# Kernel tuning notes

Hardware: AMD Instinct MI355X
Metric: run time of the kernel (lower is better)

Reference implementation:

```python
import jax, jax.numpy as jnp
import numpy as np

B, S, D, H, HD = 2, 2048, 1024, 16, 64
DFF = 4 * D
EPS = 1e-6


def _rms(x, w):
    return w * (x * jax.lax.rsqrt(jnp.mean(x * x, axis=-1, keepdims=True) + EPS))


def _rope(x, rope):
    # x: [B, H, S, HD], rope: [S, HD, 2]
    cos = rope[..., 0][None, None]
    sin = rope[..., 1][None, None]
    xr = x.reshape(*x.shape[:-1], -1, 2)
    rot = jnp.stack([-xr[..., 1], xr[..., 0]], axis=-1).reshape(x.shape)
    return x * cos + rot * sin


def setup_inputs() -> dict:
    key = jax.random.key(0)
    ks = jax.random.split(key, 10)
    w = lambda k, shape: jax.random.normal(k, shape, jnp.float32) * 0.02
    return {
        "hidden_states": jax.random.normal(ks[0], (B, S, D), jnp.float32),
        "timestep": jax.random.normal(ks[1], (B, D), jnp.float32),
        "rope_pos_embed": jax.random.normal(ks[2], (S, HD, 2), jnp.float32),
        "adaln_w": w(ks[3], (6 * D, D)),
        "adaln_b": jnp.zeros((6 * D,), jnp.float32),
        "wq": w(ks[4], (D, D)),
        "wk": w(ks[5], (D, D)),
        "wv": w(ks[6], (D, D)),
        "wo": w(ks[7], (D, D)),
        "q_norm_w": jnp.ones((D,), jnp.float32),
        "k_norm_w": jnp.ones((D,), jnp.float32),
        "norm3_w": jnp.ones((D,), jnp.float32),
        "fc1_w": w(ks[8], (DFF, D)),
        "fc1_b": jnp.zeros((DFF,), jnp.float32),
        "fc2_w": w(ks[9], (D, DFF)),
        "fc2_b": jnp.zeros((D,), jnp.float32),
    }


def reference(hidden_states, timestep, rope_pos_embed, adaln_w, adaln_b,
              wq, wk, wv, wo, q_norm_w, k_norm_w, norm3_w,
              fc1_w, fc1_b, fc2_w, fc2_b):
    x = hidden_states  # [B, S, D]
    # AdaLayerNorm: emb = Linear(SiLU(timestep)) -> 6 modulation chunks, broadcast over seq
    emb = jax.nn.silu(timestep) @ adaln_w.T + adaln_b  # [B, 6D]
    sh_msa, sc_msa, g_msa, sh_mlp, sc_mlp, g_mlp = jnp.split(emb[:, None, :], 6, axis=-1)
    mu = jnp.mean(x, axis=-1, keepdims=True)
    var = jnp.mean((x - mu) ** 2, axis=-1, keepdims=True)
    ln = (x - mu) * jax.lax.rsqrt(var + EPS)
    xm = ln * (1.0 + sc_msa) + sh_msa  # modulated input to attention

    # Attention: projections + RMSNorm over inner_dim + RoPE + SDPA
    q = _rms(xm @ wq.T, q_norm_w)
    k = _rms(xm @ wk.T, k_norm_w)
    v = xm @ wv.T
    q = q.reshape(B, S, H, HD).transpose(0, 2, 1, 3)
    k = k.reshape(B, S, H, HD).transpose(0, 2, 1, 3)
    v = v.reshape(B, S, H, HD).transpose(0, 2, 1, 3)
    q = _rope(q, rope_pos_embed)
    k = _rope(k, rope_pos_embed)
    scores = jnp.einsum('bhqd,bhkd->bhqk', q, k) * (HD ** -0.5)
    attn = jax.nn.softmax(scores, axis=-1)
    o = jnp.einsum('bhqk,bhkd->bhqd', attn, v)
    o = o.transpose(0, 2, 1, 3).reshape(B, S, H * HD) @ wo.T

    h = x + g_msa * o  # gated residual

    # MLP branch with AdaLN scale/shift on RMSNorm output
    n3 = _rms(h, norm3_w)
    nm = n3 * (1.0 + sc_mlp) + sh_mlp
    ff = jax.nn.gelu(nm @ fc1_w.T + fc1_b, approximate=True) @ fc2_w.T + fc2_b
    return h + g_mlp * ff
```

## Files before the change

kernel.cpp:

```cpp
#include <hip/hip_runtime.h>
#include <cstdint>
#include <cstddef>

typedef unsigned short ushort_t;
typedef __attribute__((ext_vector_type(8))) short s8v;
typedef __attribute__((ext_vector_type(4))) short s4v;
typedef __attribute__((ext_vector_type(4))) float f4v;

#define MFMA16(a, b, c) __builtin_amdgcn_mfma_f32_16x16x32_bf16(a, b, c, 0, 0, 0)

__device__ __forceinline__ ushort_t f2bf(float f) {
  union { float f; unsigned u; } a; a.f = f;
  return (ushort_t)((a.u + 0x7fffu + ((a.u >> 16) & 1u)) >> 16);
}
__device__ __forceinline__ float bf2f(ushort_t h) {
  union { unsigned u; float f; } a; a.u = ((unsigned)h) << 16; return a.f;
}
__device__ __forceinline__ unsigned fbits(float f) {
  union { float f; unsigned u; } a; a.f = f; return a.u;
}

__device__ __forceinline__ void gload16(const void* g, void* l) {
  __builtin_amdgcn_global_load_lds(
      (__attribute__((address_space(1))) void*)(uintptr_t)g,
      (__attribute__((address_space(3))) void*)(unsigned)(uintptr_t)l,
      16, 0, 0);
}

__launch_bounds__(256)
__global__ void convert_w(const float* __restrict__ wq, const float* __restrict__ wk,
                          const float* __restrict__ wv, const float* __restrict__ wo,
                          const float* __restrict__ f1, const float* __restrict__ f2,
                          ushort_t* __restrict__ dqkv, ushort_t* __restrict__ dwo,
                          ushort_t* __restrict__ df1, ushort_t* __restrict__ df2)
{
  const int blk = blockIdx.x;
  const float* src; ushort_t* dst; int off;
  if      (blk < 1024) { src = wq; dst = dqkv;            off = blk; }
  else if (blk < 2048) { src = wk; dst = dqkv + 1048576;  off = blk - 1024; }
  else if (blk < 3072) { src = wv; dst = dqkv + 2097152;  off = blk - 2048; }
  else if (blk < 4096) { src = wo; dst = dwo;             off = blk - 3072; }
  else if (blk < 8192) { src = f1; dst = df1;             off = blk - 4096; }
  else                 { src = f2; dst = df2;             off = blk - 8192; }
  const int idx = off * 1024 + threadIdx.x * 4;
  float4 v = *(const float4*)(src + idx);
  s4v o;
  o[0] = (short)f2bf(v.x); o[1] = (short)f2bf(v.y);
  o[2] = (short)f2bf(v.z); o[3] = (short)f2bf(v.w);
  *(s4v*)(dst + idx) = o;
}

__launch_bounds__(256)
__global__ void adaln(const float* __restrict__ ts, const float* __restrict__ w,
                      const float* __restrict__ bias, float* __restrict__ emb)
{
  const int j = blockIdx.x * 4 + (threadIdx.x >> 6);
  const int lane = threadIdx.x & 63;
  const float* wr = w + (size_t)j * 1024;
  float s0 = 0.f, s1 = 0.f;
  for (int i = lane; i < 1024; i += 64) {
    const float wv = wr[i];
    const float t0 = ts[i], t1 = ts[1024 + i];
    const float e0 = __builtin_amdgcn_exp2f(-1.4426950409f * t0);
    const float e1 = __builtin_amdgcn_exp2f(-1.4426950409f * t1);
    s0 += wv * t0 * __builtin_amdgcn_rcpf(1.f + e0);
    s1 += wv * t1 * __builtin_amdgcn_rcpf(1.f + e1);
  }
  #pragma unroll
  for (int m = 32; m; m >>= 1) { s0 += __shfl_down(s0, m); s1 += __shfl_down(s1, m); }
  if (!lane) { emb[j] = s0 + bias[j]; emb[6144 + j] = s1 + bias[j]; }
}

__launch_bounds__(256)
__global__ void ln_mod(const float* __restrict__ x, const float* __restrict__ emb,
                       ushort_t* __restrict__ xm)
{
  const int row = blockIdx.x, b = row >> 11, tid = threadIdx.x;
  const float* xr = x + (size_t)row * 1024;
  const int c = tid * 4;
  float4 v = *(const float4*)(xr + c);
  float s  = v.x + v.y + v.z + v.w;
  float s2 = v.x*v.x + v.y*v.y + v.z*v.z + v.w*v.w;
  #pragma unroll
  for (int m = 32; m; m >>= 1) { s += __shfl_down(s, m); s2 += __shfl_down(s2, m); }
  __shared__ float red[8];
  const int wave = tid >> 6, lane = tid & 63;
  if (!lane) { red[wave] = s; red[4 + wave] = s2; }
  __syncthreads();
  const float mu = (red[0] + red[1] + red[2] + red[3]) * (1.f / 1024.f);
  const float ms = (red[4] + red[5] + red[6] + red[7]) * (1.f / 1024.f);
  const float rstd = rsqrtf(ms - mu * mu + 1e-6f);
  const float* sh = emb + b * 6144;
  const float* sc = emb + b * 6144 + 1024;
  float4 shv = *(const float4*)(sh + c);
  float4 scv = *(const float4*)(sc + c);
  s4v ov;
  ov[0] = (short)f2bf((v.x - mu) * rstd * (1.f + scv.x) + shv.x);
  ov[1] = (short)f2bf((v.y - mu) * rstd * (1.f + scv.y) + shv.y);
  ov[2] = (short)f2bf((v.z - mu) * rstd * (1.f + scv.z) + shv.z);
  ov[3] = (short)f2bf((v.w - mu) * rstd * (1.f + scv.w) + shv.w);
  *(s4v*)(xm + (size_t)row * 1024 + c) = ov;
}

template<int EPI, int TN>
__launch_bounds__(256, 4)
__global__ void gemm_bt(const ushort_t* __restrict__ A, const ushort_t* __restrict__ Bw,
                        int K, int N,
                        ushort_t* __restrict__ outb, float* __restrict__ outf,
                        const float* __restrict__ bias, const float* __restrict__ resid,
                        const float* __restrict__ emb, int gate_off)
{
  constexpr int JN = TN / 32;
  constexpr int BUFB = TN * 32;
  __shared__ ushort_t As0[128 * 32], As1[128 * 32];
  __shared__ ushort_t Bs0[BUFB],    Bs1[BUFB];
  const int tid = threadIdx.x;
  const int wave = tid >> 6, lane = tid & 63;
  const int quad = lane >> 4, r = lane & 15;
  const int m0 = blockIdx.y * 128, n0 = blockIdx.x * TN;
  const int wm = (wave >> 1) * 64, wn = (wave & 1) * (TN / 2);

  const int srow = wave * 16 + (lane >> 2);
  const int scol = (lane & 3) * 8;
  const ushort_t* ag = A  + (size_t)(m0 + srow) * K + scol;
  const ushort_t* bg = Bw + (size_t)(n0 + srow) * K + scol;
  const size_t rowK64 = (size_t)64 * K;

  f4v acc[4][JN] = {};

  auto stage = [&](ushort_t* as, ushort_t* bs) {
    gload16(ag,          as + wave * 512);
    gload16(ag + rowK64, as + wave * 512 + 2048);
    gload16(bg,          bs + wave * 512);
    if (TN == 128) gload16(bg + rowK64, bs + wave * 512 + 2048);
    ag += 32; bg += 32;
  };
  auto compute = [&](const ushort_t* ab, const ushort_t* bb) {
    s8v af[4], bf[JN];
    #pragma unroll
    for (int i = 0; i < 4; i++)
      af[i] = *(const s8v*)(ab + (wm + i * 16 + r) * 32 + quad * 8);
    #pragma unroll
    for (int j = 0; j < JN; j++)
      bf[j] = *(const s8v*)(bb + (wn + j * 16 + r) * 32 + quad * 8);
    #pragma unroll
    for (int i = 0; i < 4; i++)
      #pragma unroll
      for (int j = 0; j < JN; j++)
        acc[i][j] = MFMA16(af[i], bf[j], acc[i][j]);
  };

  stage(As0, Bs0);
  __syncthreads();
  const int R = (K >> 6) - 1;
  for (int it = 0; it < R; it++) {
    stage(As1, Bs1);
    compute(As0, Bs0);
    __syncthreads();
    stage(As0, Bs0);
    compute(As1, Bs1);
    __syncthreads();
  }
  stage(As1, Bs1);
  compute(As0, Bs0);
  __syncthreads();
  compute(As1, Bs1);

  const int bblk = m0 >> 11;
  float bj[JN], gj[JN];
  #pragma unroll
  for (int j = 0; j < JN; j++) {
    const int col = n0 + wn + j * 16 + r;
    bj[j] = (EPI == 2 || EPI == 3) ? bias[col] : 0.f;
    gj[j] = (EPI == 1 || EPI == 3) ? emb[bblk * 6144 + gate_off + col] : 0.f;
  }
  #pragma unroll
  for (int i = 0; i < 4; i++) {
    #pragma unroll
    for (int rr = 0; rr < 4; rr++) {
      const int row = m0 + wm + i * 16 + quad * 4 + rr;
      const size_t rbase = (size_t)row * N + n0 + wn;
      #pragma unroll
      for (int j = 0; j < JN; j++) {
        float v = acc[i][j][rr];
        const size_t idx = rbase + j * 16 + r;
        if (EPI == 0) {
          outb[idx] = f2bf(v);
        } else if (EPI == 1) {
          outf[idx] = resid[idx] + gj[j] * v;
        } else if (EPI == 2) {
          v += bj[j];
          const float t = fmaf(v * v, 0.1029436f, 2.3022083f);
          const float e = __builtin_amdgcn_exp2f(-v * t);
          outb[idx] = f2bf(v * __builtin_amdgcn_rcpf(1.f + e));
        } else {
          outf[idx] = resid[idx] + gj[j] * (v + bj[j]);
        }
      }
    }
  }
}

__launch_bounds__(256)
__global__ void qkv_post(const ushort_t* __restrict__ qkv, const float* __restrict__ rope,
                         const float* __restrict__ qw, const float* __restrict__ kw,
                         ushort_t* __restrict__ q_r, ushort_t* __restrict__ k_r,
                         ushort_t* __restrict__ v_r)
{
  const int row = blockIdx.x, b = row >> 11, s = row & 2047, tid = threadIdx.x;
  const ushort_t* base = qkv + (size_t)row * 3072;
  const int c = tid * 4;
  s4v qv = *(const s4v*)(base + c);
  s4v kv = *(const s4v*)(base + 1024 + c);
  s4v vv = *(const s4v*)(base + 2048 + c);
  float qf[4], kf[4]; float sq = 0.f, sk = 0.f;
  #pragma unroll
  for (int i = 0; i < 4; i++) {
    qf[i] = bf2f((ushort_t)qv[i]); kf[i] = bf2f((ushort_t)kv[i]);
    sq += qf[i] * qf[i]; sk += kf[i] * kf[i];
  }
  #pragma unroll
  for (int m = 32; m; m >>= 1) { sq += __shfl_down(sq, m); sk += __shfl_down(sk, m); }
  __shared__ float red[8];
  const int wave = tid >> 6, lane = tid & 63;
  if (!lane) { red[wave] = sq; red[4 + wave] = sk; }
  __syncthreads();
  const float rq = rsqrtf((red[0]+red[1]+red[2]+red[3]) * (1.f/1024.f) + 1e-6f)
                   * 0.18033688011112042f;
  const float rk = rsqrtf((red[4]+red[5]+red[6]+red[7]) * (1.f/1024.f) + 1e-6f);

  const int h = c >> 6, d = c & 63;
  const float* rp = rope + ((size_t)s * 64 + d) * 2;
  float4 r01 = *(const float4*)(rp);
  float4 r23 = *(const float4*)(rp + 4);
  const float q0 = qf[0]*rq*qw[c], q1 = qf[1]*rq*qw[c+1];
  const float q2 = qf[2]*rq*qw[c+2], q3 = qf[3]*rq*qw[c+3];
  const float k0 = kf[0]*rk*kw[c], k1 = kf[1]*rk*kw[c+1];
  const float k2 = kf[2]*rk*kw[c+2], k3 = kf[3]*rk*kw[c+3];
  s4v qo, ko;
  qo[0] = (short)f2bf(q0 * r01.x - q1 * r01.y);
  qo[1] = (short)f2bf(q1 * r01.z + q0 * r01.w);
  qo[2] = (short)f2bf(q2 * r23.x - q3 * r23.y);
  qo[3] = (short)f2bf(q3 * r23.z + q2 * r23.w);
  ko[0] = (short)f2bf(k0 * r01.x - k1 * r01.y);
  ko[1] = (short)f2bf(k1 * r01.z + k0 * r01.w);
  ko[2] = (short)f2bf(k2 * r23.x - k3 * r23.y);
  ko[3] = (short)f2bf(k3 * r23.z + k2 * r23.w);
  const size_t rowbase = ((size_t)(b * 16 + h) * 2048 + s) * 64;
  const int d_s = (((d >> 3) ^ (s & 7)) << 3) | (d & 7);
  *(s4v*)(q_r + rowbase + d) = qo;
  *(s4v*)(k_r + rowbase + d_s) = ko;
  *(s4v*)(v_r + rowbase + d) = vv;
}

__launch_bounds__(256)
__global__ void vtrans(const ushort_t* __restrict__ v_r, ushort_t* __restrict__ v_t)
{
  const int bh = blockIdx.x >> 5, st = blockIdx.x & 31;
  const int s0 = st * 64;
  __shared__ ushort_t tile[64 * 72];
  const int tid = threadIdx.x;
  #pragma unroll
  for (int rep = 0; rep < 2; rep++) {
    const int idx = rep * 256 + tid;
    const int sr = idx >> 3, dc = (idx & 7) << 3;
    s8v val = *(const s8v*)(v_r + ((size_t)bh * 2048 + s0 + sr) * 64 + dc);
    *(s8v*)(tile + sr * 72 + dc) = val;
  }
  __syncthreads();
  #pragma unroll
  for (int rep = 0; rep < 2; rep++) {
    const int idx = rep * 256 + tid;
    const int d = idx >> 3;
    const int scs = (((idx & 7) ^ (d & 7)) << 3);
    s8v val;
    const int sc = (idx & 7) << 3;
    #pragma unroll
    for (int j = 0; j < 8; j++) val[j] = (short)tile[(sc + j) * 72 + d];
    *(s8v*)(v_t + ((size_t)bh * 64 + d) * 2048 + s0 + scs) = val;
  }
}

__launch_bounds__(256, 4)
__global__ void flash(const ushort_t* __restrict__ q_r, const ushort_t* __restrict__ k_r,
                      const ushort_t* __restrict__ v_t, ushort_t* __restrict__ attn)
{
  __shared__ ushort_t Ksh[2][64 * 64];
  __shared__ ushort_t Vsh[2][64 * 64];
  __shared__ ushort_t Psh[4][16 * 64];
  const int bh = blockIdx.x >> 5, qb = blockIdx.x & 31;
  const int tid = threadIdx.x, wave = tid >> 6, lane = tid & 63;
  const int quad = lane >> 4, r = lane & 15;
  const int rx = r & 7;
  const int q0 = qb * 64 + wave * 16;
  const size_t bhS = (size_t)bh * 2048;

  s8v aq0 = *(const s8v*)(q_r + (bhS + q0 + r) * 64 + quad * 8);
  s8v aq1 = *(const s8v*)(q_r + (bhS + q0 + r) * 64 + 32 + quad * 8);

  f4v o[4] = {};
  float mi = -1e30f, li = 0.f;

  const ushort_t* kg = k_r + (bhS + wave * 16 + (lane >> 3)) * 64 + (lane & 7) * 8;
  const ushort_t* vg = v_t + ((size_t)bh * 64 + wave * 16 + (lane >> 3)) * 2048
                       + (lane & 7) * 8;
  const int klo = wave * 1024 + lane * 8;
  const int vlo = wave * 1024 + lane * 8;
  ushort_t* pw = &Psh[wave][0];

  auto stage = [&](ushort_t* kbuf, ushort_t* vbuf, int kb) {
    #pragma unroll
    for (int c = 0; c < 2; c++) {
      gload16(kg + (size_t)(kb + c * 8) * 64, kbuf + klo + c * 512);
      gload16(vg + kb + (size_t)(c * 8) * 2048, vbuf + vlo + c * 512);
    }
  };

  auto step = [&](const ushort_t* Kc, const ushort_t* Vc) {
    f4v st[4];
    __builtin_amdgcn_s_setprio(1);
    #pragma unroll
    for (int t = 0; t < 4; t++) {
      const ushort_t* krow = Kc + (t * 16 + r) * 64;
      s8v k0 = *(const s8v*)(krow + ((quad ^ rx) << 3));
      s8v k1 = *(const s8v*)(krow + (((4 + quad) ^ rx) << 3));
      f4v z = {};
      z = MFMA16(k0, aq0, z);
      z = MFMA16(k1, aq1, z);
      st[t] = z;
    }
    __builtin_amdgcn_s_setprio(0);

    float m4[4];
    #pragma unroll
    for (int t = 0; t < 4; t++)
      m4[t] = fmaxf(fmaxf(st[t][0], st[t][1]), fmaxf(st[t][2], st[t][3]));
    float mloc = fmaxf(fmaxf(m4[0], m4[1]), fmaxf(m4[2], m4[3]));
    mloc = fmaxf(mloc, __shfl_xor(mloc, 16));
    mloc = fmaxf(mloc, __shfl_xor(mloc, 32));
    const float mn = fmaxf(mi, mloc);
    const float al = __builtin_amdgcn_exp2f(mi - mn);

    float p[4][4];
    uint2 pk[4];
    #pragma unroll
    for (int t = 0; t < 4; t++) {
      #pragma unroll
      for (int rr = 0; rr < 4; rr++)
        p[t][rr] = __builtin_amdgcn_exp2f(st[t][rr] - mn);
      const unsigned u0 = fbits(p[t][0]) + 0x8000u;
      const unsigned u1 = fbits(p[t][1]) + 0x8000u;
      const unsigned u2 = fbits(p[t][2]) + 0x8000u;
      const unsigned u3 = fbits(p[t][3]) + 0x8000u;
      pk[t].x = __builtin_amdgcn_perm(u1, u0, 0x07060302u);
      pk[t].y = __builtin_amdgcn_perm(u3, u2, 0x07060302u);
    }

    #pragma unroll
    for (int t = 0; t < 4; t++) {
      const int cw = t * 2 + (quad >> 1);
      const int sc = cw ^ rx;
      *(uint2*)(pw + r * 64 + (sc << 3) + (quad & 1) * 4) = pk[t];
    }

    float alo[4];
    #pragma unroll
    for (int rr = 0; rr < 4; rr++) alo[rr] = __shfl(al, quad * 4 + rr);
    #pragma unroll
    for (int nt = 0; nt < 4; nt++)
      #pragma unroll
      for (int rr = 0; rr < 4; rr++) o[nt][rr] *= alo[rr];

    float s4r[4];
    #pragma unroll
    for (int t = 0; t < 4; t++)
      s4r[t] = (p[t][0] + p[t][1]) + (p[t][2] + p[t][3]);
    float ls = (s4r[0] + s4r[1]) + (s4r[2] + s4r[3]);
    ls += __shfl_xor(ls, 16);
    ls += __shfl_xor(ls, 32);
    li = al * li + ls;
    mi = mn;

    asm volatile("s_waitcnt lgkmcnt(0)" ::: "memory");

    __builtin_amdgcn_s_setprio(1);
    #pragma unroll
    for (int kc = 0; kc < 2; kc++) {
      const int c = kc * 4 + quad;
      const int sc = c ^ rx;
      s8v ap = *(const s8v*)(pw + r * 64 + (sc << 3));
      #pragma unroll
      for (int nt = 0; nt < 4; nt++) {
        s8v bv = *(const s8v*)(Vc + (nt * 16 + r) * 64 + (sc << 3));
        o[nt] = MFMA16(ap, bv, o[nt]);
      }
    }
    __builtin_amdgcn_s_setprio(0);
  };

  stage(Ksh[0], Vsh[0], 0);
  __syncthreads();

  #pragma unroll 1
  for (int kb = 0; kb < 2048; kb += 128) {
    stage(Ksh[1], Vsh[1], kb + 64);
    step(Ksh[0], Vsh[0]);
    __syncthreads();
    if (kb + 128 < 2048) stage(Ksh[0], Vsh[0], kb + 128);
    step(Ksh[1], Vsh[1]);
    __syncthreads();
  }

  const int h = bh & 15, b = bh >> 4;
  const float linv = 1.f / li;
  #pragma unroll
  for (int rr = 0; rr < 4; rr++) {
    const float inv = __shfl(linv, quad * 4 + rr);
    const size_t orow = ((size_t)(b * 2048 + q0 + quad * 4 + rr)) * 1024 + h * 64;
    #pragma unroll
    for (int nt = 0; nt < 4; nt++)
      attn[orow + nt * 16 + r] = f2bf(o[nt][rr] * inv);
  }
}

__launch_bounds__(256)
__global__ void rms3_mod(const float* __restrict__ h, const float* __restrict__ emb,
                         const float* __restrict__ w3, ushort_t* __restrict__ nm)
{
  const int row = blockIdx.x, b = row >> 11, tid = threadIdx.x;
  const float* hr = h + (size_t)row * 1024;
  const int c = tid * 4;
  float4 v = *(const float4*)(hr + c);
  float s2 = v.x*v.x + v.y*v.y + v.z*v.z + v.w*v.w;
  #pragma unroll
  for (int m = 32; m; m >>= 1) s2 += __shfl_down(s2, m);
  __shared__ float red[4];
  const int wave = tid >> 6, lane = tid & 63;
  if (!lane) red[wave] = s2;
  __syncthreads();
  const float rms = rsqrtf((red[0] + red[1] + red[2] + red[3]) * (1.f / 1024.f) + 1e-6f);
  const float* sh = emb + b * 6144 + 3072;
  const float* sc = emb + b * 6144 + 4096;
  float4 shv = *(const float4*)(sh + c);
  float4 scv = *(const float4*)(sc + c);
  float4 wv  = *(const float4*)(w3 + c);
  s4v ov;
  ov[0] = (short)f2bf(v.x * rms * wv.x * (1.f + scv.x) + shv.x);
  ov[1] = (short)f2bf(v.y * rms * wv.y * (1.f + scv.y) + shv.y);
  ov[2] = (short)f2bf(v.z * rms * wv.z * (1.f + scv.z) + shv.z);
  ov[3] = (short)f2bf(v.w * rms * wv.w * (1.f + scv.w) + shv.w);
  *(s4v*)(nm + (size_t)row * 1024 + c) = ov;
}

extern "C" void kernel_launch(void* const* d_in, const int* in_sizes, int n_in,
                              void* d_out, int out_size, void* d_ws, size_t ws_size,
                              hipStream_t stream)
{
  const float* x    = (const float*)d_in[0];
  const float* ts   = (const float*)d_in[1];
  const float* rope = (const float*)d_in[2];
  const float* adw  = (const float*)d_in[3];
  const float* adb  = (const float*)d_in[4];
  const float* wq   = (const float*)d_in[5];
  const float* wk   = (const float*)d_in[6];
  const float* wv   = (const float*)d_in[7];
  const float* wo   = (const float*)d_in[8];
  const float* qnw  = (const float*)d_in[9];
  const float* knw  = (const float*)d_in[10];
  const float* n3w  = (const float*)d_in[11];
  const float* f1w  = (const float*)d_in[12];
  const float* f1b  = (const float*)d_in[13];
  const float* f2w  = (const float*)d_in[14];
  const float* f2b  = (const float*)d_in[15];

  char* ws = (char*)d_ws;
  ushort_t* WQKV = (ushort_t*)(ws + 0);
  ushort_t* WO   = (ushort_t*)(ws + 6291456);
  ushort_t* F1   = (ushort_t*)(ws + 8388608);
  ushort_t* F2   = (ushort_t*)(ws + 16777216);
  float*    EMB  = (float*)   (ws + 25165824);
  float*    H    = (float*)   (ws + 25214976);
  ushort_t* XM   = (ushort_t*)(ws + 41992192);
  ushort_t* QKV  = (ushort_t*)(ws + 50380800);
  ushort_t* QR   = (ushort_t*)(ws + 75546624);
  ushort_t* KR   = (ushort_t*)(ws + 83935232);
  ushort_t* VR   = (ushort_t*)(ws + 92323840);
  ushort_t* VT   = (ushort_t*)(ws + 100712448);
  ushort_t* ATTN = XM;
  ushort_t* NM   = QKV;
  ushort_t* FF1  = QR;

  convert_w<<<12288, 256, 0, stream>>>(wq, wk, wv, wo, f1w, f2w, WQKV, WO, F1, F2);
  adaln<<<1536, 256, 0, stream>>>(ts, adw, adb, EMB);
  ln_mod<<<4096, 256, 0, stream>>>(x, EMB, XM);
  gemm_bt<0, 128><<<dim3(24, 32), 256, 0, stream>>>(XM, WQKV, 1024, 3072,
      QKV, nullptr, nullptr, nullptr, nullptr, 0);
  qkv_post<<<4096, 256, 0, stream>>>(QKV, rope, qnw, knw, QR, KR, VR);
  vtrans<<<1024, 256, 0, stream>>>(VR, VT);
  flash<<<1024, 256, 0, stream>>>(QR, KR, VT, ATTN);
  gemm_bt<1, 64><<<dim3(16, 32), 256, 0, stream>>>(ATTN, WO, 1024, 1024,
      nullptr, H, nullptr, x, EMB, 2048);
  rms3_mod<<<4096, 256, 0, stream>>>(H, EMB, n3w, NM);
  gemm_bt<2, 128><<<dim3(32, 32), 256, 0, stream>>>(NM, F1, 1024, 4096,
      FF1, nullptr, f1b, nullptr, nullptr, 0);
  gemm_bt<3, 64><<<dim3(16, 32), 256, 0, stream>>>(FF1, F2, 4096, 1024,
      nullptr, (float*)d_out, f2b, H, EMB, 5120);
}
```

Measured before the change: 409.5 us.

## Add 256x256-tile 8-wave pipelined GEMM for QKV and FC1 projections

Adds a new GEMM kernel with 512 threads, 256x256 output tiles, double-buffered LDS staging via global_load_lds, XOR-swizzled LDS layout, wave priority hints and XCD-aware block remapping. It replaces the 128-tile GEMM for the QKV and FC1 projections. The goal is more data reuse per block, fewer blocks and better overlap of loads with MFMA work. The larger tiles use 128KB of LDS and many accumulators per thread, which may limit occupancy. With 192 and 256 blocks the grid may also underfill the GPU.

```diff
diff --git a/kernel.cpp b/kernel.cpp
--- a/kernel.cpp
+++ b/kernel.cpp
@@ -195,6 +195,143 @@
           outb[idx] = f2bf(v * __builtin_amdgcn_rcpf(1.f + e));
         } else {
           outf[idx] = resid[idx] + gj[j] * (v + bj[j]);
+        }
+      }
+    }
+  }
+}
+
+#define G8_PHASE(AB, BB, KS, MH, LOADB)                                       \
+  {                                                                           \
+    s8v af[4];                                                                \
+    const int ck = ((((KS) << 2) | quad) ^ rx) << 3;                          \
+    const ushort_t* Ap = (AB) + (wm + (MH) * 64 + r) * 64 + ck;               \
+    af[0] = *(const s8v*)(Ap);                                                \
+    af[1] = *(const s8v*)(Ap + 1024);                                         \
+    af[2] = *(const s8v*)(Ap + 2048);                                         \
+    af[3] = *(const s8v*)(Ap + 3072);                                         \
+    if (LOADB) {                                                              \
+      const ushort_t* Bp = (BB) + (wn + r) * 64 + ck;                         \
+      bf[0] = *(const s8v*)(Bp);                                              \
+      bf[1] = *(const s8v*)(Bp + 1024);                                       \
+      bf[2] = *(const s8v*)(Bp + 2048);                                       \
+      bf[3] = *(const s8v*)(Bp + 3072);                                       \
+    }                                                                         \
+    __builtin_amdgcn_s_barrier();                                             \
+    __builtin_amdgcn_s_setprio(1);                                            \
+    _Pragma("unroll")                                                         \
+    for (int i_ = 0; i_ < 4; i_++) {                                          \
+      _Pragma("unroll")                                                       \
+      for (int j_ = 0; j_ < 4; j_++)                                          \
+        acc[(MH) * 4 + i_][j_] = MFMA16(af[i_], bf[j_], acc[(MH) * 4 + i_][j_]); \
+    }                                                                         \
+    __builtin_amdgcn_s_setprio(0);                                            \
+    __builtin_amdgcn_s_barrier();                                             \
+  }
+
+template<int EPI>
+__launch_bounds__(512, 2)
+__global__ void gemm8p(const ushort_t* __restrict__ A, const ushort_t* __restrict__ Bw,
+                       int K, int N, ushort_t* __restrict__ outb,
+                       const float* __restrict__ bias)
+{
+  __shared__ ushort_t Ash[2][256 * 64];
+  __shared__ ushort_t Bsh[2][256 * 64];
+  const int tid = threadIdx.x;
+  const int wid = tid >> 6, lane = tid & 63;
+  const int quad = lane >> 4, r = lane & 15, rx = r & 7;
+
+  const int nwg = gridDim.x * gridDim.y;
+  int wg = blockIdx.y * gridDim.x + blockIdx.x;
+  wg = (wg & 7) * (nwg >> 3) + (wg >> 3);
+  const int bx = wg % gridDim.x, by = wg / gridDim.x;
+  const int m0 = by * 256, n0 = bx * 256;
+  const int wm = (wid >> 2) * 128;
+  const int wn = (wid & 3) * 64;
+
+  const int srow = lane >> 3;
+  const int scol = ((lane & 7) ^ srow) * 8;
+  const ushort_t* ag = A  + (size_t)(m0 + wid * 32 + srow) * K + scol;
+  const ushort_t* bg = Bw + (size_t)(n0 + wid * 32 + srow) * K + scol;
+  const size_t row8K = (size_t)8 * K;
+
+  f4v acc[8][4] = {};
+
+  auto STAGE = [&](int buf, int kt) {
+    const size_t ko = (size_t)kt * 64;
+    ushort_t* Ad = &Ash[buf][wid * 2048];
+    ushort_t* Bd = &Bsh[buf][wid * 2048];
+    #pragma unroll
+    for (int c = 0; c < 4; c++)
+      gload16(ag + ko + c * row8K, Ad + c * 512);
+    #pragma unroll
+    for (int c = 0; c < 4; c++)
+      gload16(bg + ko + c * row8K, Bd + c * 512);
+  };
+
+  STAGE(0, 0);
+  STAGE(1, 1);
+  asm volatile("s_waitcnt vmcnt(8)" ::: "memory");
+  __builtin_amdgcn_s_barrier();
+
+  const int NT = K >> 6;
+  #pragma unroll 1
+  for (int t = 0; t < NT; t += 2) {
+    {
+      const ushort_t* Ab = &Ash[0][0];
+      const ushort_t* Bb = &Bsh[0][0];
+      s8v bf[4];
+      G8_PHASE(Ab, Bb, 0, 0, true);
+      G8_PHASE(Ab, Bb, 0, 1, false);
+      G8_PHASE(Ab, Bb, 1, 0, true);
+      G8_PHASE(Ab, Bb, 1, 1, false);
+      if (t + 2 < NT) {
+        STAGE(0, t + 2);
+        asm volatile("s_waitcnt vmcnt(8)" ::: "memory");
+      } else {
+        asm volatile("s_waitcnt vmcnt(0)" ::: "memory");
+      }
+      __builtin_amdgcn_s_barrier();
+    }
+    {
+      const ushort_t* Ab = &Ash[1][0];
+      const ushort_t* Bb = &Bsh[1][0];
+      s8v bf[4];
+      G8_PHASE(Ab, Bb, 0, 0, true);
+      G8_PHASE(Ab, Bb, 0, 1, false);
+      G8_PHASE(Ab, Bb, 1, 0, true);
+      G8_PHASE(Ab, Bb, 1, 1, false);
+      if (t + 3 < NT) {
+        STAGE(1, t + 3);
+        asm volatile("s_waitcnt vmcnt(8)" ::: "memory");
+      } else {
+        asm volatile("s_waitcnt vmcnt(0)" ::: "memory");
+      }
+      __builtin_amdgcn_s_barrier();
+    }
+  }
+
+  float bj[4];
+  #pragma unroll
+  for (int j = 0; j < 4; j++)
+    bj[j] = (EPI == 2) ? bias[n0 + wn + j * 16 + r] : 0.f;
+  #pragma unroll
+  for (int i = 0; i < 8; i++) {
+    #pragma unroll
+    for (int rr = 0; rr < 4; rr++) {
+      const int row = m0 + wm + i * 16 + quad * 4 + rr;
+      const size_t rbase = (size_t)row * N + n0 + wn;
+      #pragma unroll
+      for (int j = 0; j < 4; j++) {
+        float v = acc[i][j][rr];
+        const size_t idx = rbase + j * 16 + r;
+        if (EPI == 0) {
+          outb[idx] = f2bf(v);
+        } else {
+          v += bj[j];
+          const float tt = fmaf(v * v, 0.1029436f, 2.3022083f);
+          const float e = __builtin_amdgcn_exp2f(-v * tt);
+          outb[idx] = f2bf(v * __builtin_amdgcn_rcpf(1.f + e));
         }
       }
     }
@@ -493,16 +630,14 @@
   convert_w<<<12288, 256, 0, stream>>>(wq, wk, wv, wo, f1w, f2w, WQKV, WO, F1, F2);
   adaln<<<1536, 256, 0, stream>>>(ts, adw, adb, EMB);
   ln_mod<<<4096, 256, 0, stream>>>(x, EMB, XM);
-  gemm_bt<0, 128><<<dim3(24, 32), 256, 0, stream>>>(XM, WQKV, 1024, 3072,
-      QKV, nullptr, nullptr, nullptr, nullptr, 0);
+  gemm8p<0><<<dim3(12, 16), 512, 0, stream>>>(XM, WQKV, 1024, 3072, QKV, nullptr);
   qkv_post<<<4096, 256, 0, stream>>>(QKV, rope, qnw, knw, QR, KR, VR);
   vtrans<<<1024, 256, 0, stream>>>(VR, VT);
   flash<<<1024, 256, 0, stream>>>(QR, KR, VT, ATTN);
   gemm_bt<1, 64><<<dim3(16, 32), 256, 0, stream>>>(ATTN, WO, 1024, 1024,
       nullptr, H, nullptr, x, EMB, 2048);
   rms3_mod<<<4096, 256, 0, stream>>>(H, EMB, n3w, NM);
-  gemm_bt<2, 128><<<dim3(32, 32), 256, 0, stream>>>(NM, F1, 1024, 4096,
-      FF1, nullptr, f1b, nullptr, nullptr, 0);
+  gemm8p<2><<<dim3(16, 16), 512, 0, stream>>>(NM, F1, 1024, 4096, FF1, f1b);
   gemm_bt<3, 64><<<dim3(16, 32), 256, 0, stream>>>(FF1, F2, 4096, 1024,
       nullptr, (float*)d_out, f2b, H, EMB, 5120);
 }
```

Measured after the change: 408.3 us. No clear change (-0.3%).
